# Optimization experiments

Measured on AMD Instinct MI355X. Metric: run time of the kernel, lower is better.

The kernel has to match this reference:

```python
import jax, jax.numpy as jnp
import numpy as np

N, M = 8192, 8192

def setup_inputs() -> dict:
    key = jax.random.key(0)
    contingency_table = jax.random.uniform(key, (N, M), dtype=jnp.float32)
    return {"contingency_table": contingency_table}

def reference(contingency_table):
    # marginals
    marginal_x = contingency_table.sum(axis=1)  # [N]
    marginal_y = contingency_table.sum(axis=0)  # [M]
    mask = contingency_table > 0
    # safe value to avoid log2(0) under the mask
    c_safe = jnp.where(mask, contingency_table, 1.0)
    denom = marginal_x[:, None] * marginal_y[None, :]  # outer product of marginals
    terms = c_safe * (jnp.log2(c_safe) - jnp.log2(denom))
    mutual_info = jnp.sum(jnp.where(mask, terms, 0.0))
    return mutual_info
```

## Files before the change

kernel.cpp:

```cpp
#include <hip/hip_runtime.h>


#define NROWS 8192
#define MCOLS 8192

__inline__ __device__ float waveReduceSum(float v) {
    #pragma unroll
    for (int off = 32; off > 0; off >>= 1)
        v += __shfl_xor(v, off, 64);
    return v;
}

__global__ __launch_bounds__(256) void mi_main(const float* __restrict__ C,
                                               float* __restrict__ P_rows,
                                               float* __restrict__ P_cols,
                                               float* __restrict__ s1_arr) {
    const int bx = blockIdx.x;
    const int by = blockIdx.y;
    const int tcol = bx * 256, trow = by * 256;
    const int tid  = threadIdx.x;
    const int lane = tid & 63;
    const int wave = tid >> 6;

    __shared__ float lds_row[256][33];
    __shared__ float lds_col[4][256];
    __shared__ float lds_s1[4];

    float c0 = 0.f, c1 = 0.f, c2 = 0.f, c3 = 0.f;
    float s1_local = 0.f;

    const float* base = C + (size_t)trow * MCOLS + tcol + lane * 4;

    #pragma unroll 4
    for (int i = 0; i < 64; ++i) {
        const int r = i * 4 + wave;
        const float4 v = *reinterpret_cast<const float4*>(base + (size_t)r * MCOLS);

        float t0 = (v.x > 0.f) ? v.x * __log2f(v.x) : 0.f;
        float t1 = (v.y > 0.f) ? v.y * __log2f(v.y) : 0.f;
        float t2 = (v.z > 0.f) ? v.z * __log2f(v.z) : 0.f;
        float t3 = (v.w > 0.f) ? v.w * __log2f(v.w) : 0.f;
        s1_local += (t0 + t1) + (t2 + t3);

        c0 += v.x; c1 += v.y; c2 += v.z; c3 += v.w;

        float p = (v.x + v.y) + (v.z + v.w);
        p += __shfl_xor(p, 32, 64);
        if (lane < 32) lds_row[r][lane] = p;
    }

    lds_col[wave][lane * 4 + 0] = c0;
    lds_col[wave][lane * 4 + 1] = c1;
    lds_col[wave][lane * 4 + 2] = c2;
    lds_col[wave][lane * 4 + 3] = c3;

    const float s1w = waveReduceSum(s1_local);
    if (lane == 0) lds_s1[wave] = s1w;

    __syncthreads();

    float rs = 0.f;
    #pragma unroll
    for (int k = 0; k < 32; ++k) rs += lds_row[tid][k];
    P_rows[(size_t)bx * NROWS + trow + tid] = rs;

    const float cs = (lds_col[0][tid] + lds_col[1][tid]) +
                     (lds_col[2][tid] + lds_col[3][tid]);
    P_cols[(size_t)by * MCOLS + tcol + tid] = cs;

    if (tid == 0)
        s1_arr[by * 32 + bx] = (lds_s1[0] + lds_s1[1]) + (lds_s1[2] + lds_s1[3]);
}

__global__ __launch_bounds__(256) void mi_ep1(const float* __restrict__ P_rows,
                                              const float* __restrict__ P_cols,
                                              const float* __restrict__ s1_arr,
                                              float* __restrict__ partials) {
    const int b    = blockIdx.x;
    const int tid  = threadIdx.x;
    const int lane = tid & 63;
    const int wave = tid >> 6;

    const float* P = (b < 32) ? P_rows : P_cols;
    const int idx  = ((b & 31) << 8) + tid;

    float x = 0.f;
    #pragma unroll
    for (int k = 0; k < 32; ++k) x += P[(size_t)k * 8192 + idx];

    float acc = (x > 0.f) ? -x * __log2f(x) : 0.f;
    if (tid < 16) acc += s1_arr[b * 16 + tid];

    acc = waveReduceSum(acc);
    __shared__ float lds[4];
    if (lane == 0) lds[wave] = acc;
    __syncthreads();
    if (tid == 0) partials[b] = (lds[0] + lds[1]) + (lds[2] + lds[3]);
}

__global__ void mi_ep2(const float* __restrict__ partials,
                       float* __restrict__ out) {
    float v = partials[threadIdx.x];
    v = waveReduceSum(v);
    if (threadIdx.x == 0) out[0] = v;
}

extern "C" void kernel_launch(void* const* d_in, const int* in_sizes, int n_in,
                              void* d_out, int out_size, void* d_ws, size_t ws_size,
                              hipStream_t stream) {
    const float* C = (const float*)d_in[0];
    float* ws      = (float*)d_ws;
    float* P_rows  = ws;
    float* P_cols  = ws + 262144;
    float* s1_arr  = ws + 524288;
    float* parts   = ws + 525312;

    dim3 grid(MCOLS / 256, NROWS / 256);
    mi_main<<<grid, 256, 0, stream>>>(C, P_rows, P_cols, s1_arr);
    mi_ep1<<<64, 256, 0, stream>>>(P_rows, P_cols, s1_arr, parts);
    mi_ep2<<<1, 64, 0, stream>>>(parts, (float*)d_out);
}
```

Measured before the change: 55.21 us.

## Fuse epilogue reductions into main kernel via last-block atomic counters

Replaces the three-kernel pipeline with one kernel. Per-row-strip and per-column-strip atomic counters let the last block in each strip finish that marginal's entropy term, and a global counter lets the final block write the result. This removes two extra kernel launches and their dependency gaps, at the cost of a memset, float atomics on one address, and a nondeterministic summation order. It also raises the main loop unroll from 4 to 8.

```diff
diff --git a/kernel.cpp b/kernel.cpp
--- a/kernel.cpp
+++ b/kernel.cpp
@@ -11,10 +11,12 @@
     return v;
 }
 
-__global__ __launch_bounds__(256) void mi_main(const float* __restrict__ C,
-                                               float* __restrict__ P_rows,
-                                               float* __restrict__ P_cols,
-                                               float* __restrict__ s1_arr) {
+__global__ __launch_bounds__(256) void mi_fused(const float* __restrict__ C,
+                                                float* __restrict__ P_rows,
+                                                float* __restrict__ P_cols,
+                                                float* __restrict__ acc,
+                                                int*   __restrict__ cnts,
+                                                float* __restrict__ out) {
     const int bx = blockIdx.x;
     const int by = blockIdx.y;
     const int tcol = bx * 256, trow = by * 256;
@@ -25,13 +27,16 @@
     __shared__ float lds_row[256][33];
     __shared__ float lds_col[4][256];
     __shared__ float lds_s1[4];
+    __shared__ float lds_red_r[4];
+    __shared__ float lds_red_c[4];
+    __shared__ int   flags;
 
     float c0 = 0.f, c1 = 0.f, c2 = 0.f, c3 = 0.f;
     float s1_local = 0.f;
 
     const float* base = C + (size_t)trow * MCOLS + tcol + lane * 4;
 
-    #pragma unroll 4
+    #pragma unroll 8
     for (int i = 0; i < 64; ++i) {
         const int r = i * 4 + wave;
         const float4 v = *reinterpret_cast<const float4*>(base + (size_t)r * MCOLS);
@@ -68,55 +73,67 @@
                      (lds_col[2][tid] + lds_col[3][tid]);
     P_cols[(size_t)by * MCOLS + tcol + tid] = cs;
 
-    if (tid == 0)
-        s1_arr[by * 32 + bx] = (lds_s1[0] + lds_s1[1]) + (lds_s1[2] + lds_s1[3]);
-}
+    __threadfence();
 
-__global__ __launch_bounds__(256) void mi_ep1(const float* __restrict__ P_rows,
-                                              const float* __restrict__ P_cols,
-                                              const float* __restrict__ s1_arr,
-                                              float* __restrict__ partials) {
-    const int b    = blockIdx.x;
-    const int tid  = threadIdx.x;
-    const int lane = tid & 63;
-    const int wave = tid >> 6;
+    if (tid == 0) {
+        atomicAdd(acc, (lds_s1[0] + lds_s1[1]) + (lds_s1[2] + lds_s1[3]));
+        int f = 0;
+        if (atomicAdd(&cnts[by], 1)      == 31) f |= 1;
+        if (atomicAdd(&cnts[32 + bx], 1) == 31) f |= 2;
+        flags = f;
+    }
+    __syncthreads();
+    const int f = flags;
 
-    const float* P = (b < 32) ? P_rows : P_cols;
-    const int idx  = ((b & 31) << 8) + tid;
+    if (f & 1) {
+        __threadfence();
+        float x = 0.f;
+        #pragma unroll
+        for (int k = 0; k < 32; ++k) x += P_rows[(size_t)k * NROWS + trow + tid];
+        float e = (x > 0.f) ? x * __log2f(x) : 0.f;
+        e = waveReduceSum(e);
+        if (lane == 0) lds_red_r[wave] = e;
+        __syncthreads();
+        if (tid == 0)
+            atomicAdd(acc, -((lds_red_r[0] + lds_red_r[1]) +
+                             (lds_red_r[2] + lds_red_r[3])));
+    }
 
-    float x = 0.f;
-    #pragma unroll
-    for (int k = 0; k < 32; ++k) x += P[(size_t)k * 8192 + idx];
+    if (f & 2) {
+        __threadfence();
+        float x = 0.f;
+        #pragma unroll
+        for (int k = 0; k < 32; ++k) x += P_cols[(size_t)k * MCOLS + tcol + tid];
+        float e = (x > 0.f) ? x * __log2f(x) : 0.f;
+        e = waveReduceSum(e);
+        if (lane == 0) lds_red_c[wave] = e;
+        __syncthreads();
+        if (tid == 0)
+            atomicAdd(acc, -((lds_red_c[0] + lds_red_c[1]) +
+                             (lds_red_c[2] + lds_red_c[3])));
+    }
 
-    float acc = (x > 0.f) ? -x * __log2f(x) : 0.f;
-    if (tid < 16) acc += s1_arr[b * 16 + tid];
-
-    acc = waveReduceSum(acc);
-    __shared__ float lds[4];
-    if (lane == 0) lds[wave] = acc;
-    __syncthreads();
-    if (tid == 0) partials[b] = (lds[0] + lds[1]) + (lds[2] + lds[3]);
-}
-
-__global__ void mi_ep2(const float* __restrict__ partials,
-                       float* __restrict__ out) {
-    float v = partials[threadIdx.x];
-    v = waveReduceSum(v);
-    if (threadIdx.x == 0) out[0] = v;
+    if (tid == 0) {
+        __threadfence();
+        if (atomicAdd(&cnts[64], 1) == 32 * 32 - 1) {
+            __threadfence();
+            out[0] = atomicAdd(acc, 0.0f);
+        }
+    }
 }
 
 extern "C" void kernel_launch(void* const* d_in, const int* in_sizes, int n_in,
                               void* d_out, int out_size, void* d_ws, size_t ws_size,
                               hipStream_t stream) {
     const float* C = (const float*)d_in[0];
-    float* ws      = (float*)d_ws;
-    float* P_rows  = ws;
-    float* P_cols  = ws + 262144;
-    float* s1_arr  = ws + 524288;
-    float* parts   = ws + 525312;
+    float* ws     = (float*)d_ws;
+    float* P_rows = ws;
+    float* P_cols = ws + 262144;
+    float* acc    = ws + 524288;
+    int*   cnts   = (int*)(ws + 524289);
+
+    hipMemsetAsync((void*)acc, 0, 512, stream);
 
     dim3 grid(MCOLS / 256, NROWS / 256);
-    mi_main<<<grid, 256, 0, stream>>>(C, P_rows, P_cols, s1_arr);
-    mi_ep1<<<64, 256, 0, stream>>>(P_rows, P_cols, s1_arr, parts);
-    mi_ep2<<<1, 64, 0, stream>>>(parts, (float*)d_out);
+    mi_fused<<<grid, 256, 0, stream>>>(C, P_rows, P_cols, acc, cnts, (float*)d_out);
 }
```

After: 178.1 us. +222.6%, slower.
